# Kernel tuning notes

Measured on AMD Instinct MI355X. Metric: run time of the kernel, lower is better.

## Reference

```python
import jax, jax.numpy as jnp
import numpy as np

EPS = 1e-8  # matches init eps


def setup_inputs() -> dict:
    key = jax.random.key(0)
    ks = jax.random.split(key, 6)
    B, LA, LB, Dh, P = 2, 512, 512, 1024, 64
    return {
        "h_a": jax.random.normal(ks[0], (B, LA, Dh), dtype=jnp.float32),
        "h_b": jax.random.normal(ks[1], (B, LB, Dh), dtype=jnp.float32),
        "Wa": jax.random.normal(ks[2], (Dh, P), dtype=jnp.float32) * 0.02,
        "ba": jax.random.normal(ks[3], (P,), dtype=jnp.float32) * 0.02,
        "Wb": jax.random.normal(ks[4], (Dh, P), dtype=jnp.float32) * 0.02,
        "bb": jax.random.normal(ks[5], (P,), dtype=jnp.float32) * 0.02,
    }


def reference(h_a, h_b, Wa, ba, Wb, bb):
    # Project + exact GELU (torch default)
    z_a = jax.nn.gelu(h_a @ Wa + ba, approximate=False)  # [B,LA,P]
    z_b = jax.nn.gelu(h_b @ Wb + bb, approximate=False)  # [B,LB,P]
    B, LA, P = z_a.shape
    LB = z_b.shape[1]
    # Channel-first broadcasts: [B,P,LA,LB]
    za = jnp.transpose(z_a, (0, 2, 1))[:, :, :, None]  # [B,P,LA,1]
    zb = jnp.transpose(z_b, (0, 2, 1))[:, :, None, :]  # [B,P,1,LB]
    za_e = jnp.broadcast_to(za, (B, P, LA, LB))
    zb_e = jnp.broadcast_to(zb, (B, P, LA, LB))
    diff = jnp.abs(za_e - zb_e)
    prod = za_e * zb_e
    # cosine similarity channel, computed from per-residue stats (no D-expanded tensor)
    dot = jnp.einsum("bip,bjp->bij", z_a, z_b)[:, None]  # [B,1,LA,LB]
    na = jnp.sqrt(jnp.sum(z_a * z_a, axis=-1) + EPS)  # [B,LA]
    nb = jnp.sqrt(jnp.sum(z_b * z_b, axis=-1) + EPS)  # [B,LB]
    sim = dot / (na[:, None, :, None] * nb[:, None, None, :])
    # channel order matches torch cat([z_a, z_b, diff, prod, sim], -1).permute(0,3,1,2)
    return jnp.concatenate([za_e, zb_e, diff, prod, sim], axis=1)  # [B,4P+1,LA,LB]
```

## Files before the change

kernel.cpp:

```cpp
#include <hip/hip_runtime.h>
#include <math.h>

#define B_    2
#define LA_   512
#define LB_   512
#define DH_   1024
#define P_    64
#define NCH_  257
#define EPS_  1e-8f
#define CH_   ((size_t)LA_ * LB_)
#define TILES_ 4
#define TROWS_ (LA_ / TILES_)

__global__ __launch_bounds__(256) void proj_gelu_kernel(
    const float* __restrict__ h_a, const float* __restrict__ Wa,
    const float* __restrict__ ba,
    const float* __restrict__ h_b, const float* __restrict__ Wb,
    const float* __restrict__ bb,
    float* __restrict__ zat,
    float* __restrict__ zbt,
    float* __restrict__ rna,
    float* __restrict__ rnb)
{
    __shared__ __align__(16) float hs[DH_];
    __shared__ float partial[256];

    const int side = blockIdx.x >> 10;
    const int row  = blockIdx.x & 1023;
    const int b    = row >> 9;
    const int i    = row & 511;
    const int tid  = threadIdx.x;

    const float* h    = side ? h_b : h_a;
    const float* W    = side ? Wb  : Wa;
    const float* bias = side ? bb  : ba;
    float* z  = side ? zbt : zat;
    float* rn = side ? rnb : rna;

    ((float4*)hs)[tid] = ((const float4*)(h + (size_t)row * DH_))[tid];
    __syncthreads();

    const int p = tid & 63;
    const int q = tid >> 6;
    const float* Wp = W + p;
    float acc = 0.f;
    const int k0 = q * 256;
    #pragma unroll 8
    for (int k = k0; k < k0 + 256; ++k)
        acc = fmaf(hs[k], Wp[k * P_], acc);
    partial[tid] = acc;
    __syncthreads();

    if (tid < 64) {
        float v = partial[tid] + partial[tid + 64] + partial[tid + 128] +
                  partial[tid + 192] + bias[tid];
        float g = 0.5f * v * (1.f + erff(v * 0.70710678118654752f));

        z[((size_t)(b * P_ + tid)) * 512 + i] = g;

        float s = g * g;
        #pragma unroll
        for (int off = 32; off > 0; off >>= 1)
            s += __shfl_down(s, off, 64);
        if (tid == 0)
            rn[row] = 1.f / sqrtf(s + EPS_);
    }
}

__global__ __launch_bounds__(256) void writer_kernel(
    const float* __restrict__ zat,
    const float* __restrict__ zbt,
    float* __restrict__ out)
{
    __shared__ __align__(16) float zbrow[LB_];
    __shared__ __align__(16) float zacol[TROWS_];

    const int ch  = blockIdx.x;
    const int t   = ch >> 6;
    const int p   = ch & 63;
    const int i0  = blockIdx.y * TROWS_;
    const int b   = blockIdx.z;
    const int tid = threadIdx.x;

    if (tid < 128)
        ((float4*)zbrow)[tid] = ((const float4*)(zbt + (size_t)(b * P_ + p) * 512))[tid];
    else if (tid < 160)
        ((float4*)zacol)[tid - 128] =
            ((const float4*)(zat + (size_t)(b * P_ + p) * 512 + i0))[tid - 128];
    __syncthreads();

    const int half = tid >> 7;
    const int jj   = (tid & 127) * 4;
    const float4 zbv = *(const float4*)(zbrow + jj);

    float* op = out + (size_t)(b * NCH_ + ch) * CH_ + (size_t)(i0 + half) * LB_ + jj;

    if (t == 0) {
        #pragma unroll 4
        for (int it = 0; it < TROWS_ / 2; ++it) {
            const float a = zacol[2 * it + half];
            *(float4*)op = make_float4(a, a, a, a);
            op += 2 * LB_;
        }
    } else if (t == 1) {
        #pragma unroll 4
        for (int it = 0; it < TROWS_ / 2; ++it) {
            *(float4*)op = make_float4(zbv.x, zbv.y, zbv.z, zbv.w);
            op += 2 * LB_;
        }
    } else if (t == 2) {
        #pragma unroll 4
        for (int it = 0; it < TROWS_ / 2; ++it) {
            const float a = zacol[2 * it + half];
            *(float4*)op = make_float4(fabsf(a - zbv.x), fabsf(a - zbv.y),
                                       fabsf(a - zbv.z), fabsf(a - zbv.w));
            op += 2 * LB_;
        }
    } else {
        #pragma unroll 4
        for (int it = 0; it < TROWS_ / 2; ++it) {
            const float a = zacol[2 * it + half];
            *(float4*)op = make_float4(a * zbv.x, a * zbv.y, a * zbv.z, a * zbv.w);
            op += 2 * LB_;
        }
    }
}

__global__ __launch_bounds__(256) void sim_kernel(
    const float* __restrict__ zat,
    const float* __restrict__ zbt,
    const float* __restrict__ rna,
    const float* __restrict__ rnb,
    float* __restrict__ out)
{
    __shared__ float zas[P_ * 16];

    const int i0  = blockIdx.x * 16;
    const int b   = blockIdx.y;
    const int tid = threadIdx.x;

    {
        const int p  = tid >> 2;
        const int ii = (tid & 3) * 4;
        *(float4*)(zas + p * 16 + ii) =
            *(const float4*)(zat + (size_t)(b * P_ + p) * 512 + i0 + ii);
    }
    __syncthreads();

    float acc0[16], acc1[16];
    #pragma unroll
    for (int ii = 0; ii < 16; ++ii) { acc0[ii] = 0.f; acc1[ii] = 0.f; }

    for (int p = 0; p < P_; ++p) {
        const float zb0 = zbt[(size_t)(b * P_ + p) * 512 + tid];
        const float zb1 = zbt[(size_t)(b * P_ + p) * 512 + tid + 256];
        #pragma unroll
        for (int ii = 0; ii < 16; ++ii) {
            const float a = zas[p * 16 + ii];
            acc0[ii] = fmaf(a, zb0, acc0[ii]);
            acc1[ii] = fmaf(a, zb1, acc1[ii]);
        }
    }

    const float rb0 = rnb[b * 512 + tid];
    const float rb1 = rnb[b * 512 + tid + 256];
    float* plane = out + (size_t)(b * NCH_ + 256) * CH_;
    #pragma unroll
    for (int ii = 0; ii < 16; ++ii) {
        const float ra = rna[b * 512 + i0 + ii];
        plane[(size_t)(i0 + ii) * LB_ + tid]       = acc0[ii] * ra * rb0;
        plane[(size_t)(i0 + ii) * LB_ + tid + 256] = acc1[ii] * ra * rb1;
    }
}

extern "C" void kernel_launch(void* const* d_in, const int* in_sizes, int n_in,
                              void* d_out, int out_size, void* d_ws, size_t ws_size,
                              hipStream_t stream)
{
    const float* h_a = (const float*)d_in[0];
    const float* h_b = (const float*)d_in[1];
    const float* Wa  = (const float*)d_in[2];
    const float* ba  = (const float*)d_in[3];
    const float* Wb  = (const float*)d_in[4];
    const float* bb  = (const float*)d_in[5];
    float* out = (float*)d_out;

    float* ws  = (float*)d_ws;
    float* zat = ws;
    float* zbt = zat + (size_t)B_ * P_ * LA_;
    float* rna = zbt + (size_t)B_ * P_ * LB_;
    float* rnb = rna + (size_t)B_ * LA_;

    proj_gelu_kernel<<<2 * B_ * LA_, 256, 0, stream>>>(
        h_a, Wa, ba, h_b, Wb, bb, zat, zbt, rna, rnb);
    writer_kernel<<<dim3(256, TILES_, B_), 256, 0, stream>>>(zat, zbt, out);
    sim_kernel<<<dim3(LA_ / 16, B_), 256, 0, stream>>>(zat, zbt, rna, rnb, out);
}
```

Baseline: 570.4 us.

## Merge writer and sim kernels into one launch with nontemporal stores

Combines the broadcast-channel writer and the cosine-similarity kernel into a single map_kernel whose grid has extra blocks for the sim plane. The sim work is re-tiled over LB into 4 column chunks so it spreads across more blocks, and all output writes use nontemporal stores to avoid polluting cache on a large streaming write. This removes one launch and the serialized tail of the sim kernel, at the cost of more divergent block types sharing one launch configuration.

```diff
diff --git a/kernel.cpp b/kernel.cpp
--- a/kernel.cpp
+++ b/kernel.cpp
@@ -12,6 +12,14 @@
 #define TILES_ 4
 #define TROWS_ (LA_ / TILES_)
 
+typedef float f32x4 __attribute__((ext_vector_type(4)));
+
+__device__ __forceinline__ void nt_store4(float* p, float x, float y, float z, float w)
+{
+    f32x4 v = {x, y, z, w};
+    __builtin_nontemporal_store(v, (f32x4*)p);
+}
+
 __global__ __launch_bounds__(256) void proj_gelu_kernel(
     const float* __restrict__ h_a, const float* __restrict__ Wa,
     const float* __restrict__ ba,
@@ -67,109 +75,105 @@
     }
 }
 
-__global__ __launch_bounds__(256) void writer_kernel(
-    const float* __restrict__ zat,
-    const float* __restrict__ zbt,
-    float* __restrict__ out)
-{
-    __shared__ __align__(16) float zbrow[LB_];
-    __shared__ __align__(16) float zacol[TROWS_];
-
-    const int ch  = blockIdx.x;
-    const int t   = ch >> 6;
-    const int p   = ch & 63;
-    const int i0  = blockIdx.y * TROWS_;
-    const int b   = blockIdx.z;
-    const int tid = threadIdx.x;
-
-    if (tid < 128)
-        ((float4*)zbrow)[tid] = ((const float4*)(zbt + (size_t)(b * P_ + p) * 512))[tid];
-    else if (tid < 160)
-        ((float4*)zacol)[tid - 128] =
-            ((const float4*)(zat + (size_t)(b * P_ + p) * 512 + i0))[tid - 128];
-    __syncthreads();
-
-    const int half = tid >> 7;
-    const int jj   = (tid & 127) * 4;
-    const float4 zbv = *(const float4*)(zbrow + jj);
-
-    float* op = out + (size_t)(b * NCH_ + ch) * CH_ + (size_t)(i0 + half) * LB_ + jj;
-
-    if (t == 0) {
-        #pragma unroll 4
-        for (int it = 0; it < TROWS_ / 2; ++it) {
-            const float a = zacol[2 * it + half];
-            *(float4*)op = make_float4(a, a, a, a);
-            op += 2 * LB_;
-        }
-    } else if (t == 1) {
-        #pragma unroll 4
-        for (int it = 0; it < TROWS_ / 2; ++it) {
-            *(float4*)op = make_float4(zbv.x, zbv.y, zbv.z, zbv.w);
-            op += 2 * LB_;
-        }
-    } else if (t == 2) {
-        #pragma unroll 4
-        for (int it = 0; it < TROWS_ / 2; ++it) {
-            const float a = zacol[2 * it + half];
-            *(float4*)op = make_float4(fabsf(a - zbv.x), fabsf(a - zbv.y),
-                                       fabsf(a - zbv.z), fabsf(a - zbv.w));
-            op += 2 * LB_;
-        }
-    } else {
-        #pragma unroll 4
-        for (int it = 0; it < TROWS_ / 2; ++it) {
-            const float a = zacol[2 * it + half];
-            *(float4*)op = make_float4(a * zbv.x, a * zbv.y, a * zbv.z, a * zbv.w);
-            op += 2 * LB_;
-        }
-    }
-}
-
-__global__ __launch_bounds__(256) void sim_kernel(
+__global__ __launch_bounds__(256) void map_kernel(
     const float* __restrict__ zat,
     const float* __restrict__ zbt,
     const float* __restrict__ rna,
     const float* __restrict__ rnb,
     float* __restrict__ out)
 {
-    __shared__ float zas[P_ * 16];
-
-    const int i0  = blockIdx.x * 16;
-    const int b   = blockIdx.y;
+    __shared__ __align__(16) float smem[P_ * 16];
+
+    const int b   = blockIdx.z;
     const int tid = threadIdx.x;
 
-    {
-        const int p  = tid >> 2;
-        const int ii = (tid & 3) * 4;
-        *(float4*)(zas + p * 16 + ii) =
-            *(const float4*)(zat + (size_t)(b * P_ + p) * 512 + i0 + ii);
-    }
-    __syncthreads();
-
-    float acc0[16], acc1[16];
-    #pragma unroll
-    for (int ii = 0; ii < 16; ++ii) { acc0[ii] = 0.f; acc1[ii] = 0.f; }
-
-    for (int p = 0; p < P_; ++p) {
-        const float zb0 = zbt[(size_t)(b * P_ + p) * 512 + tid];
-        const float zb1 = zbt[(size_t)(b * P_ + p) * 512 + tid + 256];
+    if (blockIdx.x < 256) {
+        float* zbrow = smem;
+        float* zacol = smem + LB_;
+
+        const int ch  = blockIdx.x;
+        const int t   = ch >> 6;
+        const int p   = ch & 63;
+        const int i0  = blockIdx.y * TROWS_;
+
+        if (tid < 128)
+            ((float4*)zbrow)[tid] = ((const float4*)(zbt + (size_t)(b * P_ + p) * 512))[tid];
+        else if (tid < 160)
+            ((float4*)zacol)[tid - 128] =
+                ((const float4*)(zat + (size_t)(b * P_ + p) * 512 + i0))[tid - 128];
+        __syncthreads();
+
+        const int half = tid >> 7;
+        const int jj   = (tid & 127) * 4;
+        const float4 zbv = *(const float4*)(zbrow + jj);
+
+        float* op = out + (size_t)(b * NCH_ + ch) * CH_ + (size_t)(i0 + half) * LB_ + jj;
+
+        if (t == 0) {
+            #pragma unroll 4
+            for (int it = 0; it < TROWS_ / 2; ++it) {
+                const float a = zacol[2 * it + half];
+                nt_store4(op, a, a, a, a);
+                op += 2 * LB_;
+            }
+        } else if (t == 1) {
+            #pragma unroll 4
+            for (int it = 0; it < TROWS_ / 2; ++it) {
+                nt_store4(op, zbv.x, zbv.y, zbv.z, zbv.w);
+                op += 2 * LB_;
+            }
+        } else if (t == 2) {
+            #pragma unroll 4
+            for (int it = 0; it < TROWS_ / 2; ++it) {
+                const float a = zacol[2 * it + half];
+                nt_store4(op, fabsf(a - zbv.x), fabsf(a - zbv.y),
+                              fabsf(a - zbv.z), fabsf(a - zbv.w));
+                op += 2 * LB_;
+            }
+        } else {
+            #pragma unroll 4
+            for (int it = 0; it < TROWS_ / 2; ++it) {
+                const float a = zacol[2 * it + half];
+                nt_store4(op, a * zbv.x, a * zbv.y, a * zbv.z, a * zbv.w);
+                op += 2 * LB_;
+            }
+        }
+    } else {
+        const int s  = blockIdx.x - 256;
+        const int i0 = s * 16;
+        const int j0 = blockIdx.y * 128;
+        float* zas = smem;
+
+        {
+            const int p  = tid >> 2;
+            const int i4 = (tid & 3) * 4;
+            *(float4*)(zas + p * 16 + i4) =
+                *(const float4*)(zat + (size_t)(b * P_ + p) * 512 + i0 + i4);
+        }
+        __syncthreads();
+
+        const int r = tid >> 7;
+        const int j = j0 + (tid & 127);
+
+        float acc[8];
         #pragma unroll
-        for (int ii = 0; ii < 16; ++ii) {
-            const float a = zas[p * 16 + ii];
-            acc0[ii] = fmaf(a, zb0, acc0[ii]);
-            acc1[ii] = fmaf(a, zb1, acc1[ii]);
-        }
-    }
-
-    const float rb0 = rnb[b * 512 + tid];
-    const float rb1 = rnb[b * 512 + tid + 256];
-    float* plane = out + (size_t)(b * NCH_ + 256) * CH_;
-    #pragma unroll
-    for (int ii = 0; ii < 16; ++ii) {
-        const float ra = rna[b * 512 + i0 + ii];
-        plane[(size_t)(i0 + ii) * LB_ + tid]       = acc0[ii] * ra * rb0;
-        plane[(size_t)(i0 + ii) * LB_ + tid + 256] = acc1[ii] * ra * rb1;
+        for (int u = 0; u < 8; ++u) acc[u] = 0.f;
+
+        for (int p = 0; p < P_; ++p) {
+            const float zb = zbt[(size_t)(b * P_ + p) * 512 + j];
+            #pragma unroll
+            for (int u = 0; u < 8; ++u)
+                acc[u] = fmaf(zas[p * 16 + r * 8 + u], zb, acc[u]);
+        }
+
+        const float rbj = rnb[b * 512 + j];
+        float* plane = out + (size_t)(b * NCH_ + 256) * CH_;
+        #pragma unroll
+        for (int u = 0; u < 8; ++u) {
+            const int i = i0 + r * 8 + u;
+            __builtin_nontemporal_store(acc[u] * rna[b * 512 + i] * rbj,
+                                        plane + (size_t)i * LB_ + j);
+        }
     }
 }
 
@@ -193,6 +197,6 @@
 
     proj_gelu_kernel<<<2 * B_ * LA_, 256, 0, stream>>>(
         h_a, Wa, ba, h_b, Wb, bb, zat, zbt, rna, rnb);
-    writer_kernel<<<dim3(256, TILES_, B_), 256, 0, stream>>>(zat, zbt, out);
-    sim_kernel<<<dim3(LA_ / 16, B_), 256, 0, stream>>>(zat, zbt, rna, rnb, out);
-}
+    map_kernel<<<dim3(256 + LA_ / 16, TILES_, B_), 256, 0, stream>>>(
+        zat, zbt, rna, rnb, out);
+}
```

Result: no change. 564.2 us (-1.1%).
